# Kernel optimization log

Hardware: AMD Instinct MI355X
Metric: run time of the kernel (lower is better)

## Reference

```python
import jax, jax.numpy as jnp
import numpy as np

IN_DIM, OUT_DIM = 256, 128
N_NODES, N_EDGES = 50000, 800000


def _glorot(key, shape):
    fan_in = shape[-1]
    return jax.random.normal(key, shape, dtype=jnp.float32) / jnp.sqrt(jnp.float32(fan_in))


def setup_inputs() -> dict:
    key = jax.random.key(0)
    ks = jax.random.split(key, 16)
    features1 = jax.random.normal(ks[0], (N_NODES, IN_DIM), dtype=jnp.float32)
    edge_index = jax.random.randint(ks[1], (2, N_EDGES), 0, N_NODES, dtype=jnp.int32)
    return {
        "features1": features1,
        "edge_index": edge_index,
        # encoder conv1: in->out
        "Wl_e1": _glorot(ks[2], (OUT_DIM, IN_DIM)), "bl_e1": jnp.zeros((OUT_DIM,), jnp.float32), "Wr_e1": _glorot(ks[3], (OUT_DIM, IN_DIM)),
        # encoder conv2: out->out
        "Wl_e2": _glorot(ks[4], (OUT_DIM, OUT_DIM)), "bl_e2": jnp.zeros((OUT_DIM,), jnp.float32), "Wr_e2": _glorot(ks[5], (OUT_DIM, OUT_DIM)),
        # fc: out->out
        "W_fc": _glorot(ks[6], (OUT_DIM, OUT_DIM)), "b_fc": jnp.zeros((OUT_DIM,), jnp.float32),
        # decoder conv1: out->out
        "Wl_d1": _glorot(ks[7], (OUT_DIM, OUT_DIM)), "bl_d1": jnp.zeros((OUT_DIM,), jnp.float32), "Wr_d1": _glorot(ks[8], (OUT_DIM, OUT_DIM)),
        # decoder conv2: out->in
        "Wl_d2": _glorot(ks[9], (IN_DIM, OUT_DIM)), "bl_d2": jnp.zeros((IN_DIM,), jnp.float32), "Wr_d2": _glorot(ks[10], (IN_DIM, OUT_DIM)),
    }


def _sage_conv(x, src, dst, inv_deg, Wl, bl, Wr):
    # mean aggregation of neighbor messages x[src] at destination nodes
    agg = jax.ops.segment_sum(x[src], dst, num_segments=N_NODES) * inv_deg  # [N, d_in]
    out = agg @ Wl.T + bl + x @ Wr.T  # lin_l(agg) + lin_r(x)
    # F.normalize(out, p=2, dim=-1)
    nrm = jnp.maximum(jnp.linalg.norm(out, axis=-1, keepdims=True), 1e-12)
    return out / nrm


def reference(features1, edge_index, Wl_e1, bl_e1, Wr_e1, Wl_e2, bl_e2, Wr_e2,
              W_fc, b_fc, Wl_d1, bl_d1, Wr_d1, Wl_d2, bl_d2, Wr_d2):
    src, dst = edge_index[0], edge_index[1]
    deg = jax.ops.segment_sum(jnp.ones((src.shape[0],), jnp.float32), dst, num_segments=N_NODES)
    inv_deg = (1.0 / jnp.maximum(deg, 1.0))[:, None]
    # encoder
    h = _sage_conv(features1, src, dst, inv_deg, Wl_e1, bl_e1, Wr_e1)
    x1 = _sage_conv(h, src, dst, inv_deg, Wl_e2, bl_e2, Wr_e2)
    # bottleneck linear
    x = x1 @ W_fc.T + b_fc
    # decoder
    h = _sage_conv(x, src, dst, inv_deg, Wl_d1, bl_d1, Wr_d1)
    x1_rec = _sage_conv(h, src, dst, inv_deg, Wl_d2, bl_d2, Wr_d2)
    return (x1, x1_rec)
```

## Files before the change

### kernel.cpp

```cpp
#include <hip/hip_runtime.h>
#include <hip/hip_bf16.h>
#include <math.h>

#define N_NODES 50000
#define N_EDGES 800000
#define SLOT_CAP 64
#define NB128 391
#define PREPB 2048
#define FILLA 512
#define FILLB 512
#define E_SPLIT 400000

typedef short s16x8 __attribute__((ext_vector_type(8)));
typedef float f32x4 __attribute__((ext_vector_type(4)));

static __device__ __forceinline__ unsigned short f2bf(float x) {
    __hip_bfloat16 b = __float2bfloat16(x);
    return *(unsigned short*)&b;
}
static __device__ __forceinline__ float2 bfu2f2(unsigned int u) {
    __hip_bfloat162 b = *(__hip_bfloat162*)&u;
    return __bfloat1622float2(b);
}
static __device__ __forceinline__ unsigned int packbf2(float x, float y) {
    return (unsigned int)f2bf(x) | ((unsigned int)f2bf(y) << 16);
}

#define FEATN (N_NODES * 256)
#define O_WL_E1 (FEATN)
#define O_WR_E1 (FEATN + 32768)
#define O_WL_E2 (FEATN + 65536)
#define O_WR_E2 (FEATN + 81920)
#define O_D2    (FEATN + 98304)
#define PREP_TOT (FEATN + 163840)
#define O_WD1C  (FEATN + 163840)
#define POOL_TOT (FEATN + 196608)

__global__ __launch_bounds__(256) void k_pfc(const float* __restrict__ feat,
                                             const float* __restrict__ wle1, const float* __restrict__ wre1,
                                             const float* __restrict__ wle2, const float* __restrict__ wre2,
                                             const float* __restrict__ wld2, const float* __restrict__ wrd2,
                                             const float* __restrict__ wld1, const float* __restrict__ wrd1,
                                             const float* __restrict__ wfc,  const float* __restrict__ bfc,
                                             const float* __restrict__ bld1,
                                             unsigned short* __restrict__ dstp,
                                             const int* __restrict__ esrc, const int* __restrict__ edst,
                                             int* __restrict__ cnt, int* __restrict__ slots,
                                             float* __restrict__ bT, float* __restrict__ bP) {
    if (blockIdx.x < PREPB) {
        const int tot4 = PREP_TOT / 4;
        for (int i = blockIdx.x * blockDim.x + threadIdx.x; i < tot4; i += PREPB * 256) {
            int e = i * 4;
            const float* s;
            int off;
            if      (e < O_WL_E1) { s = feat; off = e; }
            else if (e < O_WR_E1) { s = wle1; off = e - O_WL_E1; }
            else if (e < O_WL_E2) { s = wre1; off = e - O_WR_E1; }
            else if (e < O_WR_E2) { s = wle2; off = e - O_WL_E2; }
            else if (e < O_D2)    { s = wre2; off = e - O_WR_E2; }
            else {
                int rel = e - O_D2;
                int row = rel >> 8, half = (rel >> 7) & 1, col = rel & 127;
                s = half ? wrd2 : wld2;
                off = row * 128 + col;
            }
            float4 v = *(const float4*)&s[off];
            ushort4 u;
            u.x = f2bf(v.x); u.y = f2bf(v.y); u.z = f2bf(v.z); u.w = f2bf(v.w);
            *(ushort4*)&dstp[e] = u;
        }
    } else if (blockIdx.x < PREPB + FILLA) {
        const int fb = blockIdx.x - PREPB;
        for (int e = fb * 256 + threadIdx.x; e < E_SPLIT; e += FILLA * 256) {
            int d = edst[e];
            int pos = atomicAdd(&cnt[d], 1);
            if (pos < SLOT_CAP) slots[d * SLOT_CAP + pos] = esrc[e];
        }
    } else {
        const int cid = blockIdx.x - PREPB - FILLA;
        const int byy = cid / 129;
        const int bxx = cid % 129;
        const float* WX = byy ? wrd1 : wld1;
        const int t = threadIdx.x;
        if (t < 128) {
            if (bxx < 128) {
                float acc = 0.0f;
                for (int j = 0; j < 128; j++) acc += WX[bxx * 128 + j] * wfc[j * 128 + t];
                ((unsigned short*)dstp)[O_WD1C + byy * 16384 + bxx * 128 + t] = f2bf(acc);
            } else {
                float acc = 0.0f;
                for (int j = 0; j < 128; j++) acc += WX[t * 128 + j] * bfc[j];
                if (byy == 0) bT[t] = acc;
                else          bP[t] = acc + bld1[t];
            }
        }
    }
}

template <int K>
static __device__ __forceinline__ void gemm_body(int bxm, int by,
                                                 const unsigned short* __restrict__ X,
                                                 const unsigned short* __restrict__ W,
                                                 const float* __restrict__ bias0,
                                                 const float* __restrict__ bias1,
                                                 unsigned short* __restrict__ Y,
                                                 int N, int Ystride) {
    __shared__ unsigned short Ws[128 * 128];
    const unsigned short* Wsrc = W + (size_t)by * 128 * K;
    const int wid = threadIdx.x >> 6, lane = threadIdx.x & 63;
    const int row0 = bxm * 128 + wid * 32;
    const int lrow = lane & 15;
    const int lk8  = lane >> 4;
    f32x4 acc[2][8] = {};

#pragma unroll
    for (int half = 0; half < K / 128; half++) {
        if (half) __syncthreads();
        for (int idx = threadIdx.x; idx < 128 * 16; idx += 256) {
            int n = idx / 16, c = idx % 16;
            uint4 v = *(const uint4*)&Wsrc[n * K + half * 128 + c * 8];
            int cs = c ^ (n & 15);
            *(uint4*)&Ws[n * 128 + cs * 8] = v;
        }
        __syncthreads();

        const int kbase = half * 128;
        s16x8 a_cur[2];
#pragma unroll
        for (int i = 0; i < 2; i++) {
            int r = row0 + i * 16 + lrow;
            s16x8 av = {};
            if (r < N) av = *(const s16x8*)&X[(size_t)r * K + kbase + lk8 * 8];
            a_cur[i] = av;
        }
#pragma unroll
        for (int ks = 0; ks < 128; ks += 32) {
            s16x8 a_nxt[2] = {};
            if (ks + 32 < 128) {
#pragma unroll
                for (int i = 0; i < 2; i++) {
                    int r = row0 + i * 16 + lrow;
                    if (r < N) a_nxt[i] = *(const s16x8*)&X[(size_t)r * K + kbase + ks + 32 + lk8 * 8];
                }
            }
#pragma unroll
            for (int nf = 0; nf < 8; nf++) {
                int n = nf * 16 + lrow;
                int c = (ks >> 3) + lk8;
                int cs = c ^ (n & 15);
                s16x8 b = *(const s16x8*)&Ws[n * 128 + cs * 8];
                acc[0][nf] = __builtin_amdgcn_mfma_f32_16x16x32_bf16(a_cur[0], b, acc[0][nf], 0, 0, 0);
                acc[1][nf] = __builtin_amdgcn_mfma_f32_16x16x32_bf16(a_cur[1], b, acc[1][nf], 0, 0, 0);
            }
            a_cur[0] = a_nxt[0];
            a_cur[1] = a_nxt[1];
        }
    }

    const float* bias = (by == 0) ? bias0 : bias1;
    const int ccol = lane & 15, crow0 = (lane >> 4) * 4;
    const int ycol0 = by * 128;
#pragma unroll
    for (int nf = 0; nf < 8; nf++) {
        int lcol = nf * 16 + ccol;
        float bv = bias ? bias[lcol] : 0.0f;
#pragma unroll
        for (int i = 0; i < 2; i++) {
#pragma unroll
            for (int j = 0; j < 4; j++) {
                int grow = row0 + i * 16 + crow0 + j;
                if (grow < N) Y[(size_t)grow * Ystride + ycol0 + lcol] = f2bf(acc[i][nf][j] + bv);
            }
        }
    }
}

template <int K>
__global__ __launch_bounds__(256) void k_gmm2(const unsigned short* __restrict__ X,
                                              const unsigned short* __restrict__ W,
                                              const float* __restrict__ bias0,
                                              const float* __restrict__ bias1,
                                              unsigned short* __restrict__ Y,
                                              int N, int Ystride) {
    gemm_body<K>(blockIdx.x, blockIdx.y, X, W, bias0, bias1, Y, N, Ystride);
}

__global__ __launch_bounds__(256) void k_g1f(const unsigned short* __restrict__ X,
                                             const unsigned short* __restrict__ W,
                                             const float* __restrict__ bias1,
                                             unsigned short* __restrict__ Y,
                                             const int* __restrict__ esrc,
                                             const int* __restrict__ edst,
                                             int* __restrict__ cnt,
                                             int* __restrict__ slots) {
    if (blockIdx.x < 2 * NB128) {
        gemm_body<256>(blockIdx.x >> 1, blockIdx.x & 1, X, W, nullptr, bias1, Y, N_NODES, 256);
    } else {
        const int fb = blockIdx.x - 2 * NB128;
        for (int e = E_SPLIT + fb * 256 + threadIdx.x; e < N_EDGES; e += FILLB * 256) {
            int d = edst[e];
            int pos = atomicAdd(&cnt[d], 1);
            if (pos < SLOT_CAP) slots[d * SLOT_CAP + pos] = esrc[e];
        }
    }
}

__global__ __launch_bounds__(256) void k_gmmn(const unsigned short* __restrict__ X,
                                              const unsigned short* __restrict__ W,
                                              const float* __restrict__ bias,
                                              float* __restrict__ OUT, int N) {
    __shared__ unsigned short Ws[128 * 256];
    const int wid = threadIdx.x >> 6, lane = threadIdx.x & 63;
    const int row0 = blockIdx.x * 128 + wid * 32;
    const int lrow = lane & 15;
    const int lk8  = lane >> 4;
    const int ccol = lane & 15, crow0 = (lane >> 4) * 4;
    f32x4 acc[2][2][8] = {};

#pragma unroll
    for (int half = 0; half < 2; half++) {
        __syncthreads();
        const unsigned short* Wsrc = W + (size_t)half * 128 * 256;
        for (int idx = threadIdx.x; idx < 128 * 32; idx += 256) {
            int n = idx / 32, c = idx % 32;
            uint4 v = *(const uint4*)&Wsrc[n * 256 + c * 8];
            int cs = c ^ (n & 15);
            *(uint4*)&Ws[n * 256 + cs * 8] = v;
        }
        __syncthreads();

        s16x8 a_cur[2];
#pragma unroll
        for (int i = 0; i < 2; i++) {
            int r = row0 + i * 16 + lrow;
            s16x8 av = {};
            if (r < N) av = *(const s16x8*)&X[(size_t)r * 256 + lk8 * 8];
            a_cur[i] = av;
        }
#pragma unroll
        for (int ks = 0; ks < 256; ks += 32) {
            s16x8 a_nxt[2] = {};
            if (ks + 32 < 256) {
#pragma unroll
                for (int i = 0; i < 2; i++) {
                    int r = row0 + i * 16 + lrow;
                    if (r < N) a_nxt[i] = *(const s16x8*)&X[(size_t)r * 256 + ks + 32 + lk8 * 8];
                }
            }
#pragma unroll
            for (int nf = 0; nf < 8; nf++) {
                int n = nf * 16 + lrow;
                int c = (ks >> 3) + lk8;
                int cs = c ^ (n & 15);
                s16x8 b = *(const s16x8*)&Ws[n * 256 + cs * 8];
                acc[half][0][nf] = __builtin_amdgcn_mfma_f32_16x16x32_bf16(a_cur[0], b, acc[half][0][nf], 0, 0, 0);
                acc[half][1][nf] = __builtin_amdgcn_mfma_f32_16x16x32_bf16(a_cur[1], b, acc[half][1][nf], 0, 0, 0);
            }
            a_cur[0] = a_nxt[0];
            a_cur[1] = a_nxt[1];
        }
    }

#pragma unroll
    for (int half = 0; half < 2; half++)
#pragma unroll
        for (int nf = 0; nf < 8; nf++) {
            float bv = bias[half * 128 + nf * 16 + ccol];
#pragma unroll
            for (int i = 0; i < 2; i++)
#pragma unroll
                for (int j = 0; j < 4; j++) acc[half][i][nf][j] += bv;
        }
    float rs[2][4];
#pragma unroll
    for (int i = 0; i < 2; i++)
#pragma unroll
        for (int j = 0; j < 4; j++) {
            float ss = 0.0f;
#pragma unroll
            for (int half = 0; half < 2; half++)
#pragma unroll
                for (int nf = 0; nf < 8; nf++) ss += acc[half][i][nf][j] * acc[half][i][nf][j];
            ss += __shfl_xor(ss, 1); ss += __shfl_xor(ss, 2);
            ss += __shfl_xor(ss, 4); ss += __shfl_xor(ss, 8);
            rs[i][j] = 1.0f / fmaxf(sqrtf(ss), 1e-12f);
        }
#pragma unroll
    for (int i = 0; i < 2; i++)
#pragma unroll
        for (int j = 0; j < 4; j++) {
            int grow = row0 + i * 16 + crow0 + j;
            if (grow < N) {
                float r = rs[i][j];
#pragma unroll
                for (int half = 0; half < 2; half++)
#pragma unroll
                    for (int nf = 0; nf < 8; nf++)
                        OUT[(size_t)grow * 256 + half * 128 + nf * 16 + ccol] = acc[half][i][nf][j] * r;
            }
        }
}

template <bool WRITE_F32>
__global__ __launch_bounds__(256) void k_aggfin4(const uint4* __restrict__ TP,
                                                 const int* __restrict__ slots,
                                                 const int* __restrict__ cnt,
                                                 float* __restrict__ OUTF,
                                                 uint4* __restrict__ OUTB,
                                                 int ostride4, int ooff4) {
    const int wave = (blockIdx.x * blockDim.x + threadIdx.x) >> 6;
    const int lane = threadIdx.x & 63;
    if (wave >= N_NODES) return;
    const int q = lane & 15, sub = lane >> 4;
    int deg = cnt[wave];
    deg = min(deg, SLOT_CAP);
    const int base = wave * SLOT_CAP;
    float acc[8] = {};
    int i = sub * 4;
    for (; i + 3 < deg; i += 16) {
        int4 nb = *(const int4*)&slots[base + i];
        uint4 v0 = TP[(size_t)nb.x * 32 + q];
        uint4 v1 = TP[(size_t)nb.y * 32 + q];
        uint4 v2 = TP[(size_t)nb.z * 32 + q];
        uint4 v3 = TP[(size_t)nb.w * 32 + q];
        float2 a0 = bfu2f2(v0.x), a1 = bfu2f2(v0.y), a2 = bfu2f2(v0.z), a3 = bfu2f2(v0.w);
        float2 b0 = bfu2f2(v1.x), b1 = bfu2f2(v1.y), b2 = bfu2f2(v1.z), b3 = bfu2f2(v1.w);
        float2 c0 = bfu2f2(v2.x), c1 = bfu2f2(v2.y), c2 = bfu2f2(v2.z), c3 = bfu2f2(v2.w);
        float2 d0 = bfu2f2(v3.x), d1 = bfu2f2(v3.y), d2 = bfu2f2(v3.z), d3 = bfu2f2(v3.w);
        acc[0] += (a0.x + b0.x) + (c0.x + d0.x); acc[1] += (a0.y + b0.y) + (c0.y + d0.y);
        acc[2] += (a1.x + b1.x) + (c1.x + d1.x); acc[3] += (a1.y + b1.y) + (c1.y + d1.y);
        acc[4] += (a2.x + b2.x) + (c2.x + d2.x); acc[5] += (a2.y + b2.y) + (c2.y + d2.y);
        acc[6] += (a3.x + b3.x) + (c3.x + d3.x); acc[7] += (a3.y + b3.y) + (c3.y + d3.y);
    }
    const int r0 = deg & ~3;
    if (sub == ((r0 >> 2) & 3)) {
        for (int j = r0; j < deg; j++) {
            uint4 v = TP[(size_t)slots[base + j] * 32 + q];
            float2 a0 = bfu2f2(v.x), a1 = bfu2f2(v.y), a2 = bfu2f2(v.z), a3 = bfu2f2(v.w);
            acc[0] += a0.x; acc[1] += a0.y; acc[2] += a1.x; acc[3] += a1.y;
            acc[4] += a2.x; acc[5] += a2.y; acc[6] += a3.x; acc[7] += a3.y;
        }
    }
#pragma unroll
    for (int k = 0; k < 8; k++) {
        acc[k] += __shfl_xor(acc[k], 16);
        acc[k] += __shfl_xor(acc[k], 32);
    }
    const float inv = 1.0f / fmaxf((float)deg, 1.0f);
    uint4 pv = TP[(size_t)wave * 32 + 16 + q];
    float2 p0 = bfu2f2(pv.x), p1 = bfu2f2(pv.y), p2 = bfu2f2(pv.z), p3 = bfu2f2(pv.w);
    float o[8];
    o[0] = p0.x + inv * acc[0]; o[1] = p0.y + inv * acc[1];
    o[2] = p1.x + inv * acc[2]; o[3] = p1.y + inv * acc[3];
    o[4] = p2.x + inv * acc[4]; o[5] = p2.y + inv * acc[5];
    o[6] = p3.x + inv * acc[6]; o[7] = p3.y + inv * acc[7];
    float ss = 0.0f;
#pragma unroll
    for (int k = 0; k < 8; k++) ss += o[k] * o[k];
    ss += __shfl_xor(ss, 1); ss += __shfl_xor(ss, 2);
    ss += __shfl_xor(ss, 4); ss += __shfl_xor(ss, 8);
    float r = 1.0f / fmaxf(sqrtf(ss), 1e-12f);
#pragma unroll
    for (int k = 0; k < 8; k++) o[k] *= r;
    if (lane < 16) {
        if constexpr (WRITE_F32) {
            ((float4*)OUTF)[(size_t)wave * 32 + q * 2]     = make_float4(o[0], o[1], o[2], o[3]);
            ((float4*)OUTF)[(size_t)wave * 32 + q * 2 + 1] = make_float4(o[4], o[5], o[6], o[7]);
        }
        uint4 u;
        u.x = packbf2(o[0], o[1]); u.y = packbf2(o[2], o[3]);
        u.z = packbf2(o[4], o[5]); u.w = packbf2(o[6], o[7]);
        OUTB[(size_t)wave * ostride4 + ooff4 + q] = u;
    }
}

__global__ __launch_bounds__(256) void k_agg4(const uint4* __restrict__ IN,
                                              const int* __restrict__ slots,
                                              const int* __restrict__ cnt,
                                              uint4* __restrict__ OUT,
                                              int istride4, int ioff4, int ostride4, int ooff4) {
    const int wave = (blockIdx.x * blockDim.x + threadIdx.x) >> 6;
    const int lane = threadIdx.x & 63;
    if (wave >= N_NODES) return;
    const int q = lane & 15, sub = lane >> 4;
    int deg = cnt[wave];
    deg = min(deg, SLOT_CAP);
    const int base = wave * SLOT_CAP;
    float acc[8] = {};
    int i = sub * 4;
    for (; i + 3 < deg; i += 16) {
        int4 nb = *(const int4*)&slots[base + i];
        uint4 v0 = IN[(size_t)nb.x * istride4 + ioff4 + q];
        uint4 v1 = IN[(size_t)nb.y * istride4 + ioff4 + q];
        uint4 v2 = IN[(size_t)nb.z * istride4 + ioff4 + q];
        uint4 v3 = IN[(size_t)nb.w * istride4 + ioff4 + q];
        float2 a0 = bfu2f2(v0.x), a1 = bfu2f2(v0.y), a2 = bfu2f2(v0.z), a3 = bfu2f2(v0.w);
        float2 b0 = bfu2f2(v1.x), b1 = bfu2f2(v1.y), b2 = bfu2f2(v1.z), b3 = bfu2f2(v1.w);
        float2 c0 = bfu2f2(v2.x), c1 = bfu2f2(v2.y), c2 = bfu2f2(v2.z), c3 = bfu2f2(v2.w);
        float2 d0 = bfu2f2(v3.x), d1 = bfu2f2(v3.y), d2 = bfu2f2(v3.z), d3 = bfu2f2(v3.w);
        acc[0] += (a0.x + b0.x) + (c0.x + d0.x); acc[1] += (a0.y + b0.y) + (c0.y + d0.y);
        acc[2] += (a1.x + b1.x) + (c1.x + d1.x); acc[3] += (a1.y + b1.y) + (c1.y + d1.y);
        acc[4] += (a2.x + b2.x) + (c2.x + d2.x); acc[5] += (a2.y + b2.y) + (c2.y + d2.y);
        acc[6] += (a3.x + b3.x) + (c3.x + d3.x); acc[7] += (a3.y + b3.y) + (c3.y + d3.y);
    }
    const int r0 = deg & ~3;
    if (sub == ((r0 >> 2) & 3)) {
        for (int j = r0; j < deg; j++) {
            uint4 v = IN[(size_t)slots[base + j] * istride4 + ioff4 + q];
            float2 a0 = bfu2f2(v.x), a1 = bfu2f2(v.y), a2 = bfu2f2(v.z), a3 = bfu2f2(v.w);
            acc[0] += a0.x; acc[1] += a0.y; acc[2] += a1.x; acc[3] += a1.y;
            acc[4] += a2.x; acc[5] += a2.y; acc[6] += a3.x; acc[7] += a3.y;
        }
    }
#pragma unroll
    for (int k = 0; k < 8; k++) {
        acc[k] += __shfl_xor(acc[k], 16);
        acc[k] += __shfl_xor(acc[k], 32);
    }
    const float inv = 1.0f / fmaxf((float)deg, 1.0f);
    if (lane < 16) {
        uint4 u;
        u.x = packbf2(inv * acc[0], inv * acc[1]);
        u.y = packbf2(inv * acc[2], inv * acc[3]);
        u.z = packbf2(inv * acc[4], inv * acc[5]);
        u.w = packbf2(inv * acc[6], inv * acc[7]);
        OUT[(size_t)wave * ostride4 + ooff4 + q] = u;
    }
}

extern "C" void kernel_launch(void* const* d_in, const int* in_sizes, int n_in,
                              void* d_out, int out_size, void* d_ws, size_t ws_size,
                              hipStream_t stream) {
    const float* feat  = (const float*)d_in[0];
    const int*   ei    = (const int*)d_in[1];
    const int*   src   = ei;
    const int*   dst   = ei + N_EDGES;
    const float* Wl_e1 = (const float*)d_in[2];
    const float* bl_e1 = (const float*)d_in[3];
    const float* Wr_e1 = (const float*)d_in[4];
    const float* Wl_e2 = (const float*)d_in[5];
    const float* bl_e2 = (const float*)d_in[6];
    const float* Wr_e2 = (const float*)d_in[7];
    const float* W_fc  = (const float*)d_in[8];
    const float* b_fc  = (const float*)d_in[9];
    const float* Wl_d1 = (const float*)d_in[10];
    const float* bl_d1 = (const float*)d_in[11];
    const float* Wr_d1 = (const float*)d_in[12];
    const float* Wl_d2 = (const float*)d_in[13];
    const float* bl_d2 = (const float*)d_in[14];
    const float* Wr_d2 = (const float*)d_in[15];

    char* w = (char*)d_ws;
    auto alloc = [&](size_t bytes) -> void* {
        void* p = (void*)w;
        w += (bytes + 255) & ~(size_t)255;
        return p;
    };
    int* cnt   = (int*)alloc((size_t)N_NODES * 4);
    int* slots = (int*)alloc((size_t)N_NODES * SLOT_CAP * 4);
    unsigned short* bfpool = (unsigned short*)alloc((size_t)POOL_TOT * 2);
    unsigned short* TP   = (unsigned short*)alloc((size_t)N_NODES * 256 * 2);
    unsigned short* hb   = (unsigned short*)alloc((size_t)N_NODES * 128 * 2);
    unsigned short* x1b  = (unsigned short*)alloc((size_t)N_NODES * 128 * 2);
    unsigned short* X2   = (unsigned short*)alloc((size_t)N_NODES * 256 * 2);
    float* bT = (float*)alloc(128 * 4);
    float* bP = (float*)alloc(128 * 4);

    unsigned short* featb = bfpool;
    float* x1     = (float*)d_out;
    float* x1_rec = (float*)d_out + (size_t)N_NODES * 128;

    hipMemsetAsync(cnt, 0, (size_t)N_NODES * 4, stream);

    k_pfc<<<PREPB + FILLA + 258, 256, 0, stream>>>(
        feat, Wl_e1, Wr_e1, Wl_e2, Wr_e2, Wl_d2, Wr_d2,
        Wl_d1, Wr_d1, W_fc, b_fc, bl_d1,
        bfpool, src, dst, cnt, slots, bT, bP);

    const int WPB = (N_NODES * 64 + 255) / 256;

    k_g1f<<<2 * NB128 + FILLB, 256, 0, stream>>>(featb, bfpool + O_WL_E1, bl_e1, TP,
                                                 src, dst, cnt, slots);
    k_aggfin4<false><<<WPB, 256, 0, stream>>>((const uint4*)TP, slots, cnt, nullptr, (uint4*)hb, 16, 0);
    k_gmm2<128><<<dim3(NB128, 2), 256, 0, stream>>>(hb, bfpool + O_WL_E2, nullptr, bl_e2, TP, N_NODES, 256);
    k_aggfin4<true><<<WPB, 256, 0, stream>>>((const uint4*)TP, slots, cnt, x1, (uint4*)x1b, 16, 0);
    k_gmm2<128><<<dim3(NB128, 2), 256, 0, stream>>>(x1b, bfpool + O_WD1C, bT, bP, TP, N_NODES, 256);
    k_aggfin4<false><<<WPB, 256, 0, stream>>>((const uint4*)TP, slots, cnt, nullptr, (uint4*)X2, 32, 16);
    k_agg4<<<WPB, 256, 0, stream>>>((const uint4*)X2, slots, cnt, (uint4*)X2, 32, 16, 32, 0);
    k_gmmn<<<NB128, 256, 0, stream>>>(X2, bfpool + O_D2, bl_d2, x1_rec, N_NODES);
}
```

Measured before the change: 320.3 us.

## Fuse fp32-to-bf16 feature conversion into first GEMM and move edge fill there

Drops the separate pass that converted the 50000x256 fp32 feature matrix to bf16. The first-layer GEMM now reads fp32 features directly and converts them in registers before the MFMA, with a software prefetch of the next A fragment. All edge-slot filling moves into the GEMM launch, with more fill blocks, and the prep kernel shrinks to weight conversion only. This removes a large write and read of the bf16 feature copy, at the cost of the GEMM reading twice as many bytes per A element and both column blocks re-reading and re-converting the fp32 rows.

```diff
diff --git a/kernel.cpp b/kernel.cpp
--- a/kernel.cpp
+++ b/kernel.cpp
@@ -6,10 +6,7 @@
 #define N_EDGES 800000
 #define SLOT_CAP 64
 #define NB128 391
-#define PREPB 2048
-#define FILLA 512
-#define FILLB 512
-#define E_SPLIT 400000
+#define FILLB 768
 
 typedef short s16x8 __attribute__((ext_vector_type(8)));
 typedef float f32x4 __attribute__((ext_vector_type(4)));
@@ -25,59 +22,53 @@
 static __device__ __forceinline__ unsigned int packbf2(float x, float y) {
     return (unsigned int)f2bf(x) | ((unsigned int)f2bf(y) << 16);
 }
-
-#define FEATN (N_NODES * 256)
-#define O_WL_E1 (FEATN)
-#define O_WR_E1 (FEATN + 32768)
-#define O_WL_E2 (FEATN + 65536)
-#define O_WR_E2 (FEATN + 81920)
-#define O_D2    (FEATN + 98304)
-#define PREP_TOT (FEATN + 163840)
-#define O_WD1C  (FEATN + 163840)
-#define POOL_TOT (FEATN + 196608)
-
-__global__ __launch_bounds__(256) void k_pfc(const float* __restrict__ feat,
-                                             const float* __restrict__ wle1, const float* __restrict__ wre1,
-                                             const float* __restrict__ wle2, const float* __restrict__ wre2,
-                                             const float* __restrict__ wld2, const float* __restrict__ wrd2,
-                                             const float* __restrict__ wld1, const float* __restrict__ wrd1,
-                                             const float* __restrict__ wfc,  const float* __restrict__ bfc,
-                                             const float* __restrict__ bld1,
-                                             unsigned short* __restrict__ dstp,
-                                             const int* __restrict__ esrc, const int* __restrict__ edst,
-                                             int* __restrict__ cnt, int* __restrict__ slots,
-                                             float* __restrict__ bT, float* __restrict__ bP) {
-    if (blockIdx.x < PREPB) {
-        const int tot4 = PREP_TOT / 4;
-        for (int i = blockIdx.x * blockDim.x + threadIdx.x; i < tot4; i += PREPB * 256) {
-            int e = i * 4;
-            const float* s;
-            int off;
-            if      (e < O_WL_E1) { s = feat; off = e; }
-            else if (e < O_WR_E1) { s = wle1; off = e - O_WL_E1; }
-            else if (e < O_WL_E2) { s = wre1; off = e - O_WR_E1; }
-            else if (e < O_WR_E2) { s = wle2; off = e - O_WL_E2; }
-            else if (e < O_D2)    { s = wre2; off = e - O_WR_E2; }
-            else {
-                int rel = e - O_D2;
-                int row = rel >> 8, half = (rel >> 7) & 1, col = rel & 127;
-                s = half ? wrd2 : wld2;
-                off = row * 128 + col;
-            }
-            float4 v = *(const float4*)&s[off];
-            ushort4 u;
-            u.x = f2bf(v.x); u.y = f2bf(v.y); u.z = f2bf(v.z); u.w = f2bf(v.w);
-            *(ushort4*)&dstp[e] = u;
-        }
-    } else if (blockIdx.x < PREPB + FILLA) {
-        const int fb = blockIdx.x - PREPB;
-        for (int e = fb * 256 + threadIdx.x; e < E_SPLIT; e += FILLA * 256) {
-            int d = edst[e];
-            int pos = atomicAdd(&cnt[d], 1);
-            if (pos < SLOT_CAP) slots[d * SLOT_CAP + pos] = esrc[e];
-        }
+static __device__ __forceinline__ s16x8 cvt8(float4 lo, float4 hi) {
+    s16x8 r;
+    r[0] = (short)f2bf(lo.x); r[1] = (short)f2bf(lo.y);
+    r[2] = (short)f2bf(lo.z); r[3] = (short)f2bf(lo.w);
+    r[4] = (short)f2bf(hi.x); r[5] = (short)f2bf(hi.y);
+    r[6] = (short)f2bf(hi.z); r[7] = (short)f2bf(hi.w);
+    return r;
+}
+
+#define O_WL_E1 0
+#define O_WR_E1 32768
+#define O_WL_E2 65536
+#define O_WR_E2 81920
+#define O_D2    98304
+#define WPREP_TOT 163840
+#define O_WD1C  163840
+#define POOL_TOT 196608
+
+__global__ __launch_bounds__(256) void k_wc(const float* __restrict__ wle1, const float* __restrict__ wre1,
+                                            const float* __restrict__ wle2, const float* __restrict__ wre2,
+                                            const float* __restrict__ wld2, const float* __restrict__ wrd2,
+                                            const float* __restrict__ wld1, const float* __restrict__ wrd1,
+                                            const float* __restrict__ wfc,  const float* __restrict__ bfc,
+                                            const float* __restrict__ bld1,
+                                            unsigned short* __restrict__ pool,
+                                            float* __restrict__ bT, float* __restrict__ bP) {
+    if (blockIdx.x < 160) {
+        int i = blockIdx.x * 256 + threadIdx.x;
+        int e = i * 4;
+        const float* s;
+        int off;
+        if      (e < O_WR_E1)   { s = wle1; off = e - O_WL_E1; }
+        else if (e < O_WL_E2)   { s = wre1; off = e - O_WR_E1; }
+        else if (e < O_WR_E2)   { s = wle2; off = e - O_WL_E2; }
+        else if (e < O_D2)      { s = wre2; off = e - O_WR_E2; }
+        else {
+            int rel = e - O_D2;
+            int row = rel >> 8, half = (rel >> 7) & 1, col = rel & 127;
+            s = half ? wrd2 : wld2;
+            off = row * 128 + col;
+        }
+        float4 v = *(const float4*)&s[off];
+        ushort4 u;
+        u.x = f2bf(v.x); u.y = f2bf(v.y); u.z = f2bf(v.z); u.w = f2bf(v.w);
+        *(ushort4*)&pool[e] = u;
     } else {
-        const int cid = blockIdx.x - PREPB - FILLA;
+        const int cid = blockIdx.x - 160;
         const int byy = cid / 129;
         const int bxx = cid % 129;
         const float* WX = byy ? wrd1 : wld1;
@@ -86,7 +77,7 @@
             if (bxx < 128) {
                 float acc = 0.0f;
                 for (int j = 0; j < 128; j++) acc += WX[bxx * 128 + j] * wfc[j * 128 + t];
-                ((unsigned short*)dstp)[O_WD1C + byy * 16384 + bxx * 128 + t] = f2bf(acc);
+                pool[O_WD1C + byy * 16384 + bxx * 128 + t] = f2bf(acc);
             } else {
                 float acc = 0.0f;
                 for (int j = 0; j < 128; j++) acc += WX[t * 128 + j] * bfc[j];
@@ -185,7 +176,87 @@
     gemm_body<K>(blockIdx.x, blockIdx.y, X, W, bias0, bias1, Y, N, Ystride);
 }
 
-__global__ __launch_bounds__(256) void k_g1f(const unsigned short* __restrict__ X,
+static __device__ __forceinline__ void gemm_body_e1(int bxm, int by,
+                                                    const float* __restrict__ X,
+                                                    const unsigned short* __restrict__ W,
+                                                    const float* __restrict__ bias1,
+                                                    unsigned short* __restrict__ Y) {
+    __shared__ unsigned short Ws[128 * 128];
+    const unsigned short* Wsrc = W + (size_t)by * 128 * 256;
+    const int wid = threadIdx.x >> 6, lane = threadIdx.x & 63;
+    const int row0 = bxm * 128 + wid * 32;
+    const int lrow = lane & 15;
+    const int lk8  = lane >> 4;
+    f32x4 acc[2][8] = {};
+
+#pragma unroll
+    for (int half = 0; half < 2; half++) {
+        if (half) __syncthreads();
+        for (int idx = threadIdx.x; idx < 128 * 16; idx += 256) {
+            int n = idx / 16, c = idx % 16;
+            uint4 v = *(const uint4*)&Wsrc[n * 256 + half * 128 + c * 8];
+            int cs = c ^ (n & 15);
+            *(uint4*)&Ws[n * 128 + cs * 8] = v;
+        }
+        __syncthreads();
+
+        const int kbase = half * 128;
+        s16x8 a_cur[2];
+#pragma unroll
+        for (int i = 0; i < 2; i++) {
+            int r = row0 + i * 16 + lrow;
+            s16x8 av = {};
+            if (r < N_NODES) {
+                const float* xp = &X[(size_t)r * 256 + kbase + lk8 * 8];
+                av = cvt8(*(const float4*)xp, *(const float4*)(xp + 4));
+            }
+            a_cur[i] = av;
+        }
+#pragma unroll
+        for (int ks = 0; ks < 128; ks += 32) {
+            s16x8 a_nxt[2] = {};
+            if (ks + 32 < 128) {
+#pragma unroll
+                for (int i = 0; i < 2; i++) {
+                    int r = row0 + i * 16 + lrow;
+                    if (r < N_NODES) {
+                        const float* xp = &X[(size_t)r * 256 + kbase + ks + 32 + lk8 * 8];
+                        a_nxt[i] = cvt8(*(const float4*)xp, *(const float4*)(xp + 4));
+                    }
+                }
+            }
+#pragma unroll
+            for (int nf = 0; nf < 8; nf++) {
+                int n = nf * 16 + lrow;
+                int c = (ks >> 3) + lk8;
+                int cs = c ^ (n & 15);
+                s16x8 b = *(const s16x8*)&Ws[n * 128 + cs * 8];
+                acc[0][nf] = __builtin_amdgcn_mfma_f32_16x16x32_bf16(a_cur[0], b, acc[0][nf], 0, 0, 0);
+                acc[1][nf] = __builtin_amdgcn_mfma_f32_16x16x32_bf16(a_cur[1], b, acc[1][nf], 0, 0, 0);
+            }
+            a_cur[0] = a_nxt[0];
+            a_cur[1] = a_nxt[1];
+        }
+    }
+
+    const int ccol = lane & 15, crow0 = (lane >> 4) * 4;
+    const int ycol0 = by * 128;
+#pragma unroll
+    for (int nf = 0; nf < 8; nf++) {
+        int lcol = nf * 16 + ccol;
+        float bv = by ? bias1[lcol] : 0.0f;
+#pragma unroll
+        for (int i = 0; i < 2; i++) {
+#pragma unroll
+            for (int j = 0; j < 4; j++) {
+                int grow = row0 + i * 16 + crow0 + j;
+                if (grow < N_NODES) Y[(size_t)grow * 256 + ycol0 + lcol] = f2bf(acc[i][nf][j] + bv);
+            }
+        }
+    }
+}
+
+__global__ __launch_bounds__(256) void k_g1f(const float* __restrict__ X,
                                              const unsigned short* __restrict__ W,
                                              const float* __restrict__ bias1,
                                              unsigned short* __restrict__ Y,
@@ -194,10 +265,10 @@
                                              int* __restrict__ cnt,
                                              int* __restrict__ slots) {
     if (blockIdx.x < 2 * NB128) {
-        gemm_body<256>(blockIdx.x >> 1, blockIdx.x & 1, X, W, nullptr, bias1, Y, N_NODES, 256);
+        gemm_body_e1(blockIdx.x >> 1, blockIdx.x & 1, X, W, bias1, Y);
     } else {
         const int fb = blockIdx.x - 2 * NB128;
-        for (int e = E_SPLIT + fb * 256 + threadIdx.x; e < N_EDGES; e += FILLB * 256) {
+        for (int e = fb * 256 + threadIdx.x; e < N_EDGES; e += FILLB * 256) {
             int d = edst[e];
             int pos = atomicAdd(&cnt[d], 1);
             if (pos < SLOT_CAP) slots[d * SLOT_CAP + pos] = esrc[e];
@@ -458,7 +529,7 @@
     };
     int* cnt   = (int*)alloc((size_t)N_NODES * 4);
     int* slots = (int*)alloc((size_t)N_NODES * SLOT_CAP * 4);
-    unsigned short* bfpool = (unsigned short*)alloc((size_t)POOL_TOT * 2);
+    unsigned short* pool = (unsigned short*)alloc((size_t)POOL_TOT * 2);
     unsigned short* TP   = (unsigned short*)alloc((size_t)N_NODES * 256 * 2);
     unsigned short* hb   = (unsigned short*)alloc((size_t)N_NODES * 128 * 2);
     unsigned short* x1b  = (unsigned short*)alloc((size_t)N_NODES * 128 * 2);
@@ -466,26 +537,23 @@
     float* bT = (float*)alloc(128 * 4);
     float* bP = (float*)alloc(128 * 4);
 
-    unsigned short* featb = bfpool;
     float* x1     = (float*)d_out;
     float* x1_rec = (float*)d_out + (size_t)N_NODES * 128;
 
     hipMemsetAsync(cnt, 0, (size_t)N_NODES * 4, stream);
 
-    k_pfc<<<PREPB + FILLA + 258, 256, 0, stream>>>(
-        feat, Wl_e1, Wr_e1, Wl_e2, Wr_e2, Wl_d2, Wr_d2,
-        Wl_d1, Wr_d1, W_fc, b_fc, bl_d1,
-        bfpool, src, dst, cnt, slots, bT, bP);
+    k_wc<<<160 + 258, 256, 0, stream>>>(Wl_e1, Wr_e1, Wl_e2, Wr_e2, Wl_d2, Wr_d2,
+                                        Wl_d1, Wr_d1, W_fc, b_fc, bl_d1, pool, bT, bP);
 
     const int WPB = (N_NODES * 64 + 255) / 256;
 
-    k_g1f<<<2 * NB128 + FILLB, 256, 0, stream>>>(featb, bfpool + O_WL_E1, bl_e1, TP,
+    k_g1f<<<2 * NB128 + FILLB, 256, 0, stream>>>(feat, pool + O_WL_E1, bl_e1, TP,
                                                  src, dst, cnt, slots);
     k_aggfin4<false><<<WPB, 256, 0, stream>>>((const uint4*)TP, slots, cnt, nullptr, (uint4*)hb, 16, 0);
-    k_gmm2<128><<<dim3(NB128, 2), 256, 0, stream>>>(hb, bfpool + O_WL_E2, nullptr, bl_e2, TP, N_NODES, 256);
+    k_gmm2<128><<<dim3(NB128, 2), 256, 0, stream>>>(hb, pool + O_WL_E2, nullptr, bl_e2, TP, N_NODES, 256);
     k_aggfin4<true><<<WPB, 256, 0, stream>>>((const uint4*)TP, slots, cnt, x1, (uint4*)x1b, 16, 0);
-    k_gmm2<128><<<dim3(NB128, 2), 256, 0, stream>>>(x1b, bfpool + O_WD1C, bT, bP, TP, N_NODES, 256);
+    k_gmm2<128><<<dim3(NB128, 2), 256, 0, stream>>>(x1b, pool + O_WD1C, bT, bP, TP, N_NODES, 256);
     k_aggfin4<false><<<WPB, 256, 0, stream>>>((const uint4*)TP, slots, cnt, nullptr, (uint4*)X2, 32, 16);
     k_agg4<<<WPB, 256, 0, stream>>>((const uint4*)X2, slots, cnt, (uint4*)X2, 32, 16, 32, 0);
-    k_gmmn<<<NB128, 256, 0, stream>>>(X2, bfpool + O_D2, bl_d2, x1_rec, N_NODES);
-}
+    k_gmmn<<<NB128, 256, 0, stream>>>(X2, pool + O_D2, bl_d2, x1_rec, N_NODES);
+}
```

New measurement: 306.1 us (median of 2 runs). -4.4%, faster.
